# Performance work log

Hardware: AMD Instinct MI355X
Metric: run time of the kernel (lower is better)

The kernel has to match this reference:

```python
import jax, jax.numpy as jnp
import numpy as np

N = 16384
MUL0, MUL1, MUL2 = 128, 64, 32            # multiplicities of 0e, 1e, 2e
A = 16                                    # node_attr_dim (Ax0e)
D0, D1, D2 = MUL0, MUL1 * 3, MUL2 * 5     # e3nn flat block sizes
DIN = D0 + D1 + D2                        # 480
NGATE = MUL1 + MUL2                       # 96 gate scalars
OUT0 = MUL0 + NGATE                       # 224 scalar (0e) outputs of fctp_1


def setup_inputs() -> dict:
    key = jax.random.key(0)
    ks = jax.random.split(key, 10)
    f32 = jnp.float32
    return {
        "node_vec": jax.random.normal(ks[0], (N, DIN), f32),
        "node_embedding": jax.random.normal(ks[1], (N, A), f32),
        # fctp_1 path weights (fully-connected TP with Ax0e attr)
        "W1_l0": jax.random.normal(ks[2], (MUL0, A, OUT0), f32),
        "W1_l1": jax.random.normal(ks[3], (MUL1, A, MUL1), f32),
        "W1_l2": jax.random.normal(ks[4], (MUL2, A, MUL2), f32),
        "b1": jnp.zeros((OUT0,), f32),
        # fctp_2 scalar-path weight (only 0e x 0e -> 0e path exists)
        "W2": jax.random.normal(ks[5], (MUL0, A, A), f32),
        "b2": jnp.zeros((A,), f32),
        # scalar readout MLP: LinearRS -> SiLU -> LinearRS
        "W3": jax.random.normal(ks[6], (A, A), f32),
        "b3": jnp.zeros((A,), f32),
        "W4": jax.random.normal(ks[7], (A, 1), f32),
        "b4": jnp.zeros((1,), f32),
    }


def reference(node_vec, node_embedding, W1_l0, W1_l1, W1_l2, b1, W2, b2, W3, b3, W4, b4):
    # split e3nn-layout features into per-l blocks [N, mul, 2l+1]
    x0 = node_vec[:, :D0]                               # [N, 128]   l=0
    x1 = node_vec[:, D0:D0 + D1].reshape(-1, MUL1, 3)   # [N, 64, 3] l=1
    x2 = node_vec[:, D0 + D1:].reshape(-1, MUL2, 5)     # [N, 32, 5] l=2
    a = node_embedding                                  # [N, A] 0e scalars
    # fctp_1: fully-connected TP with Ax0e attr -> per-l bilinear mix (path-normalized)
    s = jnp.einsum('ni,na,iak->nk', x0, a, W1_l0) / np.sqrt(MUL0 * A) + b1  # [N, 224]
    y1 = jnp.einsum('nim,na,iak->nkm', x1, a, W1_l1) / np.sqrt(MUL1 * A)    # [N, 64, 3]
    y2 = jnp.einsum('nim,na,iak->nkm', x2, a, W1_l2) / np.sqrt(MUL2 * A)    # [N, 32, 5]
    # SwishGate: SiLU on scalars, sigmoid gates multiply the l>0 channels
    scalars = jax.nn.silu(s[:, :MUL0])
    gates = jax.nn.sigmoid(s[:, MUL0:])
    y1 = y1 * gates[:, :MUL1, None]
    y2 = y2 * gates[:, MUL1:, None]
    # fctp_2: output irreps = Ax0e, so only the 0e x 0e -> 0e path exists;
    # the gated l>0 features have no path to 0e (same as the torch TP).
    mid = jnp.einsum('ni,na,iak->nk', scalars, a, W2) / np.sqrt(MUL0 * A) + b2  # [N, A]
    # output_network: LinearRS -> SiLU -> LinearRS (rescale 1/sqrt(fan_in))
    h = jax.nn.silu(mid @ W3 / np.sqrt(A) + b3)
    return h @ W4 / np.sqrt(A) + b4                     # [N, 1]
```

## Files before the change

### kernel.cpp

```cpp
#include <hip/hip_runtime.h>


#define NKC 64

typedef _Float16 h8 __attribute__((ext_vector_type(8)));
typedef _Float16 h2 __attribute__((ext_vector_type(2)));
typedef float    f32x4 __attribute__((ext_vector_type(4)));
typedef unsigned int u32;

static __device__ __forceinline__ u32 pack2h(float a, float b) {
    h2 t = {(_Float16)a, (_Float16)b};
    return __builtin_bit_cast(u32, t);
}
static __device__ __forceinline__ f32x4 mfma_h(uint4 a, uint4 b, f32x4 c) {
    return __builtin_amdgcn_mfma_f32_16x16x32_f16(
        __builtin_bit_cast(h8, a), __builtin_bit_cast(h8, b), c, 0, 0, 0);
}
static __device__ __forceinline__ uint4 mk_afrag(_Float16 xh, const h2* ee) {
    h2 xx = {xh, xh};
    uint4 r;
    r.x = __builtin_bit_cast(u32, (h2)(xx * ee[0]));
    r.y = __builtin_bit_cast(u32, (h2)(xx * ee[1]));
    r.z = __builtin_bit_cast(u32, (h2)(xx * ee[2]));
    r.w = __builtin_bit_cast(u32, (h2)(xx * ee[3]));
    return r;
}

__global__ __launch_bounds__(256) void prep_kernel(
        const float* __restrict__ W1, const float* __restrict__ W2,
        _Float16* __restrict__ W1T, _Float16* __restrict__ W2T) {
    const int b = blockIdx.x, kc = b >> 2, tp = b & 3;
    const int tid = threadIdx.x;
    __shared__ float l1[32 * 36];
    __shared__ float l2[32 * 20];

    {
        int row = tid >> 3, c4 = tid & 7;
        float4 v = *(const float4*)(W1 + (size_t)(kc * 32 + row) * 224 + tp * 32 + c4 * 4);
        *(float4*)(l1 + row * 36 + c4 * 4) = v;
    }
    if (tp == 0 && tid < 128) {
        int row = tid >> 2, c4 = tid & 3;
        float4 v = *(const float4*)(W2 + (size_t)(kc * 32 + row) * 16 + c4 * 4);
        *(float4*)(l2 + row * 20 + c4 * 4) = v;
    }
    __syncthreads();

    if (tid < 128) {
        int tl = tid >> 6, t = tp * 2 + tl, lane = tid & 63;
        int q = lane >> 4, cc = lane & 15, colL = tl * 16 + cc;
        u32 w[4];
#pragma unroll
        for (int jj = 0; jj < 4; ++jj)
            w[jj] = pack2h(l1[(q * 8 + 2 * jj) * 36 + colL],
                           l1[(q * 8 + 2 * jj + 1) * 36 + colL]);
        *(uint4*)(W1T + (size_t)kc * 4096 + (t * 64 + lane) * 8) =
            make_uint4(w[0], w[1], w[2], w[3]);
    }
    if (tp == 0 && tid >= 128 && tid < 192) {
        int lane = tid - 128, q = lane >> 4, cc = lane & 15;
        u32 w[4];
#pragma unroll
        for (int jj = 0; jj < 4; ++jj)
            w[jj] = pack2h(l2[(q * 8 + 2 * jj) * 20 + cc],
                           l2[(q * 8 + 2 * jj + 1) * 20 + cc]);
        *(uint4*)(W2T + (size_t)kc * 512 + lane * 8) = make_uint4(w[0], w[1], w[2], w[3]);
    }
}

__global__ __launch_bounds__(512, 2) void main_kernel(
        const float* __restrict__ node_vec, const float* __restrict__ emb,
        const _Float16* __restrict__ W1T, const _Float16* __restrict__ W2T,
        const float* __restrict__ b1, const float* __restrict__ b2,
        const float* __restrict__ W3, const float* __restrict__ b3,
        const float* __restrict__ W4, const float* __restrict__ b4,
        float* __restrict__ out) {
    __shared__ _Float16 xe[64 * 72];
    __shared__ _Float16 xo[64 * 72];
    __shared__ float    midp[4 * 64 * 17];
    __shared__ float    mids[64 * 17];
    __shared__ float    w3s[256];
    __shared__ float    b3s[16];
    __shared__ float    w4s[16];
    __shared__ float    b4s[1];

    const int tid  = threadIdx.x;
    const int wave = tid >> 6, lane = tid & 63;
    const int q = lane >> 4, c = lane & 15;
    const int ih = q >> 1;
    const int aodd = q & 1;
    const int nodeBase = blockIdx.x * 64;

    for (int idx = tid; idx < 2048; idx += 512) {
        int row = idx >> 5, c4 = idx & 31;
        float4 v = *(const float4*)(node_vec + (size_t)(nodeBase + row) * 480 + c4 * 4);
        h2 ev = {(_Float16)v.x, (_Float16)v.z};
        h2 ov = {(_Float16)v.y, (_Float16)v.w};
        *(h2*)(xe + row * 72 + c4 * 2) = ev;
        *(h2*)(xo + row * 72 + c4 * 2) = ov;
    }
    if (tid < 256) w3s[tid] = W3[tid];
    if (tid < 16) { b3s[tid] = b3[tid]; w4s[tid] = W4[tid]; }
    if (tid == 0) b4s[0] = b4[0];

    h2 eeg[4][4];
#pragma unroll
    for (int g = 0; g < 4; ++g) {
        const float* ep = emb + (size_t)(nodeBase + g * 16 + c) * 16 + aodd * 8;
        float4 v0 = *(const float4*)ep;
        float4 v1 = *(const float4*)(ep + 4);
        eeg[g][0] = (h2){(_Float16)v0.x, (_Float16)v0.y};
        eeg[g][1] = (h2){(_Float16)v0.z, (_Float16)v0.w};
        eeg[g][2] = (h2){(_Float16)v1.x, (_Float16)v1.y};
        eeg[g][3] = (h2){(_Float16)v1.z, (_Float16)v1.w};
    }
    __syncthreads();

    f32x4 acc[4];
#pragma unroll
    for (int g = 0; g < 4; ++g) acc[g] = (f32x4){0.f, 0.f, 0.f, 0.f};

    const int t = wave;
    const uint4* bp = (const uint4*)W1T + t * 64 + lane;
    const _Float16* xbase = (ih ? xo : xe);
    const _Float16* xrow0 = xbase + (0 * 16 + c) * 72;
    const _Float16* xrow1 = xbase + (1 * 16 + c) * 72;
    const _Float16* xrow2 = xbase + (2 * 16 + c) * 72;
    const _Float16* xrow3 = xbase + (3 * 16 + c) * 72;

    uint4 ring[8];
#pragma unroll
    for (int r = 0; r < 8; ++r) ring[r] = bp[r * 512];
    h2 xh2[4];
    xh2[0] = *(const h2*)xrow0; xh2[1] = *(const h2*)xrow1;
    xh2[2] = *(const h2*)xrow2; xh2[3] = *(const h2*)xrow3;

#pragma unroll 8
    for (int kc = 0; kc < NKC; ++kc) {
        uint4 cur = ring[kc & 7];
        if (kc + 8 < NKC) ring[kc & 7] = bp[(kc + 8) * 512];
        _Float16 xv0 = xh2[0][kc & 1], xv1 = xh2[1][kc & 1];
        _Float16 xv2 = xh2[2][kc & 1], xv3 = xh2[3][kc & 1];
        if ((kc & 1) && kc + 1 < NKC) {
            int nx = kc + 1;
            xh2[0] = *(const h2*)(xrow0 + nx); xh2[1] = *(const h2*)(xrow1 + nx);
            xh2[2] = *(const h2*)(xrow2 + nx); xh2[3] = *(const h2*)(xrow3 + nx);
        }
        acc[0] = mfma_h(mk_afrag(xv0, eeg[0]), cur, acc[0]);
        acc[1] = mfma_h(mk_afrag(xv1, eeg[1]), cur, acc[1]);
        acc[2] = mfma_h(mk_afrag(xv2, eeg[2]), cur, acc[2]);
        acc[3] = mfma_h(mk_afrag(xv3, eeg[3]), cur, acc[3]);
    }

    __syncthreads();

    const float inv2048 = 0.022097086912079608f;
    {
        float bb1v = b1[t * 16 + c];
        _Float16* dst = (c & 1) ? xo : xe;
        int colh = t * 8 + (c >> 1);
#pragma unroll
        for (int g = 0; g < 4; ++g) {
#pragma unroll
            for (int r = 0; r < 4; ++r) {
                int node = g * 16 + q * 4 + r;
                float s  = acc[g][r] * inv2048 + bb1v;
                float sc = s / (1.f + __expf(-s));
                dst[node * 72 + colh] = (_Float16)sc;
            }
        }
    }
    __syncthreads();

    {
        const int nh = wave >> 2, ks = wave & 3;
        const _Float16* sbase = (ih ? xo : xe);
        const _Float16* srow0 = sbase + ((nh * 2 + 0) * 16 + c) * 72 + ks * 16;
        const _Float16* srow1 = sbase + ((nh * 2 + 1) * 16 + c) * 72 + ks * 16;
        h8 s0a = *(const h8*)srow0, s0b = *(const h8*)(srow0 + 8);
        h8 s1a = *(const h8*)srow1, s1b = *(const h8*)(srow1 + 8);
        const uint4* b2p = (const uint4*)W2T + lane;
        f32x4 m0 = (f32x4){0.f, 0.f, 0.f, 0.f};
        f32x4 m1 = (f32x4){0.f, 0.f, 0.f, 0.f};
        uint4 wb[4];
#pragma unroll
        for (int u = 0; u < 4; ++u) wb[u] = b2p[(ks * 16 + u) * 64];
#pragma unroll
        for (int k2 = 0; k2 < 16; ++k2) {
            uint4 cur = wb[k2 & 3];
            if (k2 + 4 < 16) wb[k2 & 3] = b2p[(ks * 16 + k2 + 4) * 64];
            _Float16 sv0 = (k2 < 8) ? s0a[k2] : s0b[k2 - 8];
            _Float16 sv1 = (k2 < 8) ? s1a[k2] : s1b[k2 - 8];
            m0 = mfma_h(mk_afrag(sv0, eeg[nh * 2 + 0]), cur, m0);
            m1 = mfma_h(mk_afrag(sv1, eeg[nh * 2 + 1]), cur, m1);
        }
#pragma unroll
        for (int r = 0; r < 4; ++r) {
            int n0 = (nh * 2 + 0) * 16 + q * 4 + r;
            int n1 = (nh * 2 + 1) * 16 + q * 4 + r;
            midp[(ks * 64 + n0) * 17 + c] = m0[r];
            midp[(ks * 64 + n1) * 17 + c] = m1[r];
        }
    }
    __syncthreads();

    {
        int n0 = tid >> 4, col = tid & 15;
#pragma unroll
        for (int half = 0; half < 2; ++half) {
            int node = n0 + half * 32;
            float m = midp[node * 17 + col] + midp[(64 + node) * 17 + col]
                    + midp[(128 + node) * 17 + col] + midp[(192 + node) * 17 + col];
            mids[node * 17 + col] = m * inv2048 + b2[col];
        }
    }
    __syncthreads();

    {
        int n0 = tid >> 4, jj = tid & 15;
#pragma unroll
        for (int half = 0; half < 2; ++half) {
            int n = n0 + half * 32;
            float a = 0.f;
#pragma unroll
            for (int cc = 0; cc < 16; ++cc) a += mids[n * 17 + cc] * w3s[cc * 16 + jj];
            a = a * 0.25f + b3s[jj];
            float hh = a / (1.f + __expf(-a));
            float po = hh * w4s[jj];
            po += __shfl_xor(po, 1);
            po += __shfl_xor(po, 2);
            po += __shfl_xor(po, 4);
            po += __shfl_xor(po, 8);
            if (jj == 0) out[nodeBase + n] = po * 0.25f + b4s[0];
        }
    }
}

extern "C" void kernel_launch(void* const* d_in, const int* in_sizes, int n_in,
                              void* d_out, int out_size, void* d_ws, size_t ws_size,
                              hipStream_t stream) {
    const float* node_vec = (const float*)d_in[0];
    const float* emb      = (const float*)d_in[1];
    const float* W1       = (const float*)d_in[2];
    const float* b1v      = (const float*)d_in[5];
    const float* W2       = (const float*)d_in[6];
    const float* b2v      = (const float*)d_in[7];
    const float* W3       = (const float*)d_in[8];
    const float* b3v      = (const float*)d_in[9];
    const float* W4       = (const float*)d_in[10];
    const float* b4v      = (const float*)d_in[11];

    _Float16* W1T = (_Float16*)d_ws;
    _Float16* W2T = W1T + 64 * 4096;
    float* out = (float*)d_out;

    prep_kernel<<<256, 256, 0, stream>>>(W1, W2, W1T, W2T);
    main_kernel<<<256, 512, 0, stream>>>(node_vec, emb, W1T, W2T,
                                         b1v, b2v, W3, b3v, W4, b4v, out);
}
```

Before: 113.2 us.

## Split K across two wave groups with 1024-thread blocks and LDS reduction

The block grows from 512 to 1024 threads so the 64-step fctp_1 K loop is split between two groups of 8 waves, each doing 32 steps. The second group writes its partial accumulators to shared memory and the first adds them before the SiLU. The fctp_2 and readout stages are redistributed so each wave or thread handles one node group, which removes the second per-thread iteration. The goal is to halve the serial MFMA and weight-load chain per wave and give each CU more waves to hide latency. In exchange it adds an extra shared-memory reduction and sync, and uses more LDS per block, which limits residency to one block per CU.

```diff
diff --git a/kernel.cpp b/kernel.cpp
--- a/kernel.cpp
+++ b/kernel.cpp
@@ -1,7 +1,5 @@
 #include <hip/hip_runtime.h>
 
-
-#define NKC 64
 
 typedef _Float16 h8 __attribute__((ext_vector_type(8)));
 typedef _Float16 h2 __attribute__((ext_vector_type(2)));
@@ -68,21 +66,25 @@
     }
 }
 
-__global__ __launch_bounds__(512, 2) void main_kernel(
+__global__ __launch_bounds__(1024) void main_kernel(
         const float* __restrict__ node_vec, const float* __restrict__ emb,
         const _Float16* __restrict__ W1T, const _Float16* __restrict__ W2T,
         const float* __restrict__ b1, const float* __restrict__ b2,
         const float* __restrict__ W3, const float* __restrict__ b3,
         const float* __restrict__ W4, const float* __restrict__ b4,
         float* __restrict__ out) {
-    __shared__ _Float16 xe[64 * 72];
-    __shared__ _Float16 xo[64 * 72];
-    __shared__ float    midp[4 * 64 * 17];
-    __shared__ float    mids[64 * 17];
-    __shared__ float    w3s[256];
-    __shared__ float    b3s[16];
-    __shared__ float    w4s[16];
-    __shared__ float    b4s[1];
+    __shared__ __align__(16) _Float16 xsh[2 * 4608 + 8];
+    __shared__ __align__(16) char     uni[32768];
+    __shared__ float w3s[256];
+    __shared__ float b3s[16];
+    __shared__ float w4s[16];
+    __shared__ float b4s[1];
+
+    _Float16* xe  = xsh;
+    _Float16* xo  = xsh + 4608 + 8;
+    float*    part = (float*)uni;
+    float*    midp = (float*)uni;
+    float*    mids = (float*)(uni + 17408);
 
     const int tid  = threadIdx.x;
     const int wave = tid >> 6, lane = tid & 63;
@@ -91,7 +93,7 @@
     const int aodd = q & 1;
     const int nodeBase = blockIdx.x * 64;
 
-    for (int idx = tid; idx < 2048; idx += 512) {
+    for (int idx = tid; idx < 2048; idx += 1024) {
         int row = idx >> 5, c4 = idx & 31;
         float4 v = *(const float4*)(node_vec + (size_t)(nodeBase + row) * 480 + c4 * 4);
         h2 ev = {(_Float16)v.x, (_Float16)v.z};
@@ -116,55 +118,68 @@
     }
     __syncthreads();
 
+    const int kh = wave >> 3;
+    const int t  = wave & 7;
     f32x4 acc[4];
 #pragma unroll
     for (int g = 0; g < 4; ++g) acc[g] = (f32x4){0.f, 0.f, 0.f, 0.f};
 
-    const int t = wave;
-    const uint4* bp = (const uint4*)W1T + t * 64 + lane;
-    const _Float16* xbase = (ih ? xo : xe);
-    const _Float16* xrow0 = xbase + (0 * 16 + c) * 72;
-    const _Float16* xrow1 = xbase + (1 * 16 + c) * 72;
-    const _Float16* xrow2 = xbase + (2 * 16 + c) * 72;
-    const _Float16* xrow3 = xbase + (3 * 16 + c) * 72;
+    const uint4* bp = (const uint4*)W1T + t * 64 + lane + kh * 32 * 512;
+    const _Float16* xb = (ih ? xo : xe) + kh * 32;
+    const _Float16* xr0 = xb + (0 * 16 + c) * 72;
+    const _Float16* xr1 = xb + (1 * 16 + c) * 72;
+    const _Float16* xr2 = xb + (2 * 16 + c) * 72;
+    const _Float16* xr3 = xb + (3 * 16 + c) * 72;
 
     uint4 ring[8];
 #pragma unroll
     for (int r = 0; r < 8; ++r) ring[r] = bp[r * 512];
-    h2 xh2[4];
-    xh2[0] = *(const h2*)xrow0; xh2[1] = *(const h2*)xrow1;
-    xh2[2] = *(const h2*)xrow2; xh2[3] = *(const h2*)xrow3;
-
-#pragma unroll 8
-    for (int kc = 0; kc < NKC; ++kc) {
-        uint4 cur = ring[kc & 7];
-        if (kc + 8 < NKC) ring[kc & 7] = bp[(kc + 8) * 512];
-        _Float16 xv0 = xh2[0][kc & 1], xv1 = xh2[1][kc & 1];
-        _Float16 xv2 = xh2[2][kc & 1], xv3 = xh2[3][kc & 1];
-        if ((kc & 1) && kc + 1 < NKC) {
-            int nx = kc + 1;
-            xh2[0] = *(const h2*)(xrow0 + nx); xh2[1] = *(const h2*)(xrow1 + nx);
-            xh2[2] = *(const h2*)(xrow2 + nx); xh2[3] = *(const h2*)(xrow3 + nx);
-        }
-        acc[0] = mfma_h(mk_afrag(xv0, eeg[0]), cur, acc[0]);
-        acc[1] = mfma_h(mk_afrag(xv1, eeg[1]), cur, acc[1]);
-        acc[2] = mfma_h(mk_afrag(xv2, eeg[2]), cur, acc[2]);
-        acc[3] = mfma_h(mk_afrag(xv3, eeg[3]), cur, acc[3]);
-    }
-
+    h8 xcur[4], xnxt[4];
+    xcur[0] = *(const h8*)xr0;       xcur[1] = *(const h8*)xr1;
+    xcur[2] = *(const h8*)xr2;       xcur[3] = *(const h8*)xr3;
+    xnxt[0] = *(const h8*)(xr0 + 8); xnxt[1] = *(const h8*)(xr1 + 8);
+    xnxt[2] = *(const h8*)(xr2 + 8); xnxt[3] = *(const h8*)(xr3 + 8);
+
+#pragma unroll
+    for (int bb = 0; bb < 4; ++bb) {
+#pragma unroll
+        for (int u = 0; u < 8; ++u) {
+            const int kl = bb * 8 + u;
+            uint4 cur = ring[u];
+            ring[u] = bp[(kl + 8) * 512];
+            acc[0] = mfma_h(mk_afrag(xcur[0][u], eeg[0]), cur, acc[0]);
+            acc[1] = mfma_h(mk_afrag(xcur[1][u], eeg[1]), cur, acc[1]);
+            acc[2] = mfma_h(mk_afrag(xcur[2][u], eeg[2]), cur, acc[2]);
+            acc[3] = mfma_h(mk_afrag(xcur[3][u], eeg[3]), cur, acc[3]);
+        }
+        xcur[0] = xnxt[0]; xcur[1] = xnxt[1];
+        xcur[2] = xnxt[2]; xcur[3] = xnxt[3];
+        if (bb + 2 < 4) {
+            const int o = (bb + 2) * 8;
+            xnxt[0] = *(const h8*)(xr0 + o); xnxt[1] = *(const h8*)(xr1 + o);
+            xnxt[2] = *(const h8*)(xr2 + o); xnxt[3] = *(const h8*)(xr3 + o);
+        }
+    }
+
+    if (kh == 1) {
+#pragma unroll
+        for (int g = 0; g < 4; ++g)
+            *(f32x4*)(part + (t * 16 + c) * 64 + g * 16 + q * 4) = acc[g];
+    }
     __syncthreads();
 
     const float inv2048 = 0.022097086912079608f;
-    {
+    if (kh == 0) {
         float bb1v = b1[t * 16 + c];
         _Float16* dst = (c & 1) ? xo : xe;
         int colh = t * 8 + (c >> 1);
 #pragma unroll
         for (int g = 0; g < 4; ++g) {
+            f32x4 p = *(const f32x4*)(part + (t * 16 + c) * 64 + g * 16 + q * 4);
 #pragma unroll
             for (int r = 0; r < 4; ++r) {
                 int node = g * 16 + q * 4 + r;
-                float s  = acc[g][r] * inv2048 + bb1v;
+                float s  = (acc[g][r] + p[r]) * inv2048 + bb1v;
                 float sc = s / (1.f + __expf(-s));
                 dst[node * 72 + colh] = (_Float16)sc;
             }
@@ -173,15 +188,11 @@
     __syncthreads();
 
     {
-        const int nh = wave >> 2, ks = wave & 3;
-        const _Float16* sbase = (ih ? xo : xe);
-        const _Float16* srow0 = sbase + ((nh * 2 + 0) * 16 + c) * 72 + ks * 16;
-        const _Float16* srow1 = sbase + ((nh * 2 + 1) * 16 + c) * 72 + ks * 16;
-        h8 s0a = *(const h8*)srow0, s0b = *(const h8*)(srow0 + 8);
-        h8 s1a = *(const h8*)srow1, s1b = *(const h8*)(srow1 + 8);
+        const int ng = wave >> 2, ks = wave & 3;
+        const _Float16* srow = (ih ? xo : xe) + (ng * 16 + c) * 72 + ks * 16;
+        h8 sa = *(const h8*)srow, sb = *(const h8*)(srow + 8);
         const uint4* b2p = (const uint4*)W2T + lane;
         f32x4 m0 = (f32x4){0.f, 0.f, 0.f, 0.f};
-        f32x4 m1 = (f32x4){0.f, 0.f, 0.f, 0.f};
         uint4 wb[4];
 #pragma unroll
         for (int u = 0; u < 4; ++u) wb[u] = b2p[(ks * 16 + u) * 64];
@@ -189,50 +200,38 @@
         for (int k2 = 0; k2 < 16; ++k2) {
             uint4 cur = wb[k2 & 3];
             if (k2 + 4 < 16) wb[k2 & 3] = b2p[(ks * 16 + k2 + 4) * 64];
-            _Float16 sv0 = (k2 < 8) ? s0a[k2] : s0b[k2 - 8];
-            _Float16 sv1 = (k2 < 8) ? s1a[k2] : s1b[k2 - 8];
-            m0 = mfma_h(mk_afrag(sv0, eeg[nh * 2 + 0]), cur, m0);
-            m1 = mfma_h(mk_afrag(sv1, eeg[nh * 2 + 1]), cur, m1);
+            _Float16 sv = (k2 < 8) ? sa[k2] : sb[k2 - 8];
+            m0 = mfma_h(mk_afrag(sv, eeg[ng]), cur, m0);
         }
 #pragma unroll
         for (int r = 0; r < 4; ++r) {
-            int n0 = (nh * 2 + 0) * 16 + q * 4 + r;
-            int n1 = (nh * 2 + 1) * 16 + q * 4 + r;
-            midp[(ks * 64 + n0) * 17 + c] = m0[r];
-            midp[(ks * 64 + n1) * 17 + c] = m1[r];
-        }
-    }
-    __syncthreads();
-
-    {
-        int n0 = tid >> 4, col = tid & 15;
-#pragma unroll
-        for (int half = 0; half < 2; ++half) {
-            int node = n0 + half * 32;
-            float m = midp[node * 17 + col] + midp[(64 + node) * 17 + col]
-                    + midp[(128 + node) * 17 + col] + midp[(192 + node) * 17 + col];
-            mids[node * 17 + col] = m * inv2048 + b2[col];
-        }
-    }
-    __syncthreads();
-
-    {
-        int n0 = tid >> 4, jj = tid & 15;
-#pragma unroll
-        for (int half = 0; half < 2; ++half) {
-            int n = n0 + half * 32;
-            float a = 0.f;
-#pragma unroll
-            for (int cc = 0; cc < 16; ++cc) a += mids[n * 17 + cc] * w3s[cc * 16 + jj];
-            a = a * 0.25f + b3s[jj];
-            float hh = a / (1.f + __expf(-a));
-            float po = hh * w4s[jj];
-            po += __shfl_xor(po, 1);
-            po += __shfl_xor(po, 2);
-            po += __shfl_xor(po, 4);
-            po += __shfl_xor(po, 8);
-            if (jj == 0) out[nodeBase + n] = po * 0.25f + b4s[0];
-        }
+            int node = ng * 16 + q * 4 + r;
+            midp[(ks * 64 + node) * 17 + c] = m0[r];
+        }
+    }
+    __syncthreads();
+
+    {
+        int node = tid >> 4, col = tid & 15;
+        float m = midp[node * 17 + col] + midp[(64 + node) * 17 + col]
+                + midp[(128 + node) * 17 + col] + midp[(192 + node) * 17 + col];
+        mids[node * 17 + col] = m * inv2048 + b2[col];
+    }
+    __syncthreads();
+
+    {
+        int n = tid >> 4, jj = tid & 15;
+        float a = 0.f;
+#pragma unroll
+        for (int cc = 0; cc < 16; ++cc) a += mids[n * 17 + cc] * w3s[cc * 16 + jj];
+        a = a * 0.25f + b3s[jj];
+        float hh = a / (1.f + __expf(-a));
+        float po = hh * w4s[jj];
+        po += __shfl_xor(po, 1);
+        po += __shfl_xor(po, 2);
+        po += __shfl_xor(po, 4);
+        po += __shfl_xor(po, 8);
+        if (jj == 0) out[nodeBase + n] = po * 0.25f + b4s[0];
     }
 }
 
@@ -255,6 +254,6 @@
     float* out = (float*)d_out;
 
     prep_kernel<<<256, 256, 0, stream>>>(W1, W2, W1T, W2T);
-    main_kernel<<<256, 512, 0, stream>>>(node_vec, emb, W1T, W2T,
-                                         b1v, b2v, W3, b3v, W4, b4v, out);
-}
+    main_kernel<<<256, 1024, 0, stream>>>(node_vec, emb, W1T, W2T,
+                                          b1v, b2v, W3, b3v, W4, b4v, out);
+}
```

Result: no change. 111.9 us (-1.1%).
